# Optimization experiments

Hardware: AMD Instinct MI355X
Metric: run time of the kernel (lower is better)

The kernel has to match this reference:

```python
import jax, jax.numpy as jnp
import numpy as np

N_HEAD = 16
LN_EPS = 1e-5


def _layernorm(x, g, b):
    mu = jnp.mean(x, axis=-1, keepdims=True)
    var = jnp.mean(jnp.square(x - mu), axis=-1, keepdims=True)
    return (x - mu) * jax.lax.rsqrt(var + LN_EPS) * g + b


def setup_inputs() -> dict:
    key = jax.random.key(0)
    ks = jax.random.split(key, 8)
    B, T, C = 2, 2048, 1024
    Dff = 4 * C
    s = 0.02
    return {
        "x": jax.random.normal(ks[0], (B, T, C), jnp.float32),
        "wq": jax.random.normal(ks[1], (C, C), jnp.float32) * s,
        "wk": jax.random.normal(ks[2], (C, C), jnp.float32) * s,
        "wv": jax.random.normal(ks[3], (C, C), jnp.float32) * s,
        "w_proj": jax.random.normal(ks[4], (C, C), jnp.float32) * s,
        "b_proj": jnp.zeros((C,), jnp.float32),
        "w1": jax.random.normal(ks[5], (C, Dff), jnp.float32) * s,
        "b1": jnp.zeros((Dff,), jnp.float32),
        "w2": jax.random.normal(ks[6], (Dff, C), jnp.float32) * s,
        "b2": jnp.zeros((C,), jnp.float32),
        "g1": jnp.ones((C,), jnp.float32),
        "be1": jnp.zeros((C,), jnp.float32),
        "g2": jnp.ones((C,), jnp.float32),
        "be2": jnp.zeros((C,), jnp.float32),
    }


def reference(x, wq, wk, wv, w_proj, b_proj, w1, b1, w2, b2, g1, be1, g2, be2):
    B, T, C = x.shape
    H = N_HEAD
    hd = C // H
    # QKV projections (all heads folded into one matmul each), -> [B,H,T,hd]
    q = (x @ wq).reshape(B, T, H, hd).transpose(0, 2, 1, 3)
    k = (x @ wk).reshape(B, T, H, hd).transpose(0, 2, 1, 3)
    v = (x @ wv).reshape(B, T, H, hd).transpose(0, 2, 1, 3)
    # scaled causal attention; scale = head_size ** -0.5 as in torch source
    scores = jnp.einsum("bhqd,bhkd->bhqk", q, k) * (hd ** -0.5)
    causal = jnp.tril(jnp.ones((T, T), bool))
    scores = jnp.where(causal, scores, jnp.finfo(scores.dtype).min)
    wei = jax.nn.softmax(scores, axis=-1)
    attn = jnp.einsum("bhqk,bhkd->bhqd", wei, v)  # [B,H,T,hd]
    attn = attn.transpose(0, 2, 1, 3).reshape(B, T, C)
    y = attn @ w_proj + b_proj
    # post-LN residuals as in Block.forward
    x = _layernorm(x + y, g1, be1)
    y = jnp.maximum(x @ w1 + b1, 0.0) @ w2 + b2
    x = _layernorm(x + y, g2, be2)
    return x
```

## Files before the change

kernel.cpp:

```cpp
#include <hip/hip_runtime.h>
#include <hip/hip_bf16.h>


typedef __attribute__((ext_vector_type(8))) short bf16x8;
typedef __attribute__((ext_vector_type(4))) float f32x4;
typedef __attribute__((ext_vector_type(4))) short short4v;

__device__ inline short f2bf(float f) {
    __hip_bfloat16 h = __float2bfloat16(f);
    return *reinterpret_cast<short*>(&h);
}
__device__ inline float bf2f(short s) {
    union { unsigned u; float f; } c;
    c.u = ((unsigned)(unsigned short)s) << 16;
    return c.f;
}

__global__ __launch_bounds__(256) void mega_prep(const float* __restrict__ x,
                                                 short* __restrict__ x_bf,
                                                 const float* __restrict__ wq,
                                                 const float* __restrict__ wk,
                                                 const float* __restrict__ wv,
                                                 const float* __restrict__ wp,
                                                 short* __restrict__ wqT,
                                                 short* __restrict__ wkT,
                                                 short* __restrict__ wvT,
                                                 short* __restrict__ wpT,
                                                 const float* __restrict__ w1,
                                                 short* __restrict__ w1T,
                                                 const float* __restrict__ w2,
                                                 short* __restrict__ w2T,
                                                 float scaleq) {
    const int blk = blockIdx.x;
    const int tid = threadIdx.x;
    if (blk < 4096) {
        const int i = blk * 256 + tid;
        float4 v = *(const float4*)(x + (size_t)i * 4);
        short4v o = { f2bf(v.x), f2bf(v.y), f2bf(v.z), f2bf(v.w) };
        *(short4v*)(x_bf + (size_t)i * 4) = o;
        return;
    }
    __shared__ short tile[32][33];
    const int tx = tid & 31, ty = tid >> 5;
    const float* in;
    short* out;
    int R, C, bx, by;
    float scale = 1.0f;
    if (blk < 8192) {
        const int b2 = blk - 4096;
        const int z = b2 >> 10;
        const int rem = b2 & 1023;
        bx = rem & 31; by = rem >> 5;
        R = 1024; C = 1024;
        in = z == 0 ? wq : z == 1 ? wk : z == 2 ? wv : wp;
        out = z == 0 ? wqT : z == 1 ? wkT : z == 2 ? wvT : wpT;
        if (z == 0) scale = scaleq;
    } else if (blk < 12288) {
        const int rem = blk - 8192;
        bx = rem & 127; by = rem >> 7;
        R = 1024; C = 4096;
        in = w1; out = w1T;
    } else {
        const int rem = blk - 12288;
        bx = rem & 31; by = rem >> 5;
        R = 4096; C = 1024;
        in = w2; out = w2T;
    }
    const int c0 = bx * 32, r0 = by * 32;
    for (int i = ty; i < 32; i += 8)
        tile[i][tx] = f2bf(in[(size_t)(r0 + i) * C + c0 + tx] * scale);
    __syncthreads();
    for (int i = ty; i < 32; i += 8)
        out[(size_t)(c0 + i) * R + r0 + tx] = tile[tx][i];
}

template <int BN, int BIAS, int RELU, int OUTBF>
__device__ __forceinline__ void gemm_core(const short* __restrict__ A,
                                          const short* __restrict__ BT,
                                          const float* __restrict__ bias,
                                          void* __restrict__ Cout,
                                          int N, int K, int lda, int ldb,
                                          int gx, int w,
                                          short* As, short* Bs, bool addbias) {
    constexpr int NI = BN / 32;
    const int tid = threadIdx.x;
    const int wid = tid >> 6;
    const int lane = tid & 63;
    const int wr = wid >> 1, wc = wid & 1;
    const int row0 = (w % gx) * 128;
    const int col0 = (w / gx) * BN;
    const int lr = lane & 15;
    const int lk = (lane >> 4) * 8;
    const int sr = lane >> 3;
    const int scs = ((lane & 7) * 8) ^ (sr * 8);
    const int rsw = (lr & 7) * 8;

    f32x4 acc[4][NI] = {};
    for (int k = 0; k < K; k += 64) {
#pragma unroll
        for (int c = 0; c < 4; ++c) {
            const int ch = wid + c * 4;
            const short* ga = A + (size_t)(row0 + ch * 8 + sr) * lda + k + scs;
            __builtin_amdgcn_global_load_lds(
                (const __attribute__((address_space(1))) unsigned int*)ga,
                (__attribute__((address_space(3))) unsigned int*)(As + ch * 512), 16, 0, 0);
        }
#pragma unroll
        for (int c = 0; c < BN / 32; ++c) {
            const int ch = wid + c * 4;
            const short* gb = BT + (size_t)(col0 + ch * 8 + sr) * ldb + k + scs;
            __builtin_amdgcn_global_load_lds(
                (const __attribute__((address_space(1))) unsigned int*)gb,
                (__attribute__((address_space(3))) unsigned int*)(Bs + ch * 512), 16, 0, 0);
        }
        __syncthreads();
#pragma unroll
        for (int kk = 0; kk < 64; kk += 32) {
            const int cof = (kk + lk) ^ rsw;
            bf16x8 a[4], b[NI];
#pragma unroll
            for (int m = 0; m < 4; ++m)
                a[m] = *(const bf16x8*)(As + (wr * 64 + m * 16 + lr) * 64 + cof);
#pragma unroll
            for (int n = 0; n < NI; ++n)
                b[n] = *(const bf16x8*)(Bs + (wc * (BN / 2) + n * 16 + lr) * 64 + cof);
#pragma unroll
            for (int m = 0; m < 4; ++m)
#pragma unroll
                for (int n = 0; n < NI; ++n)
                    acc[m][n] = __builtin_amdgcn_mfma_f32_16x16x32_bf16(a[m], b[n], acc[m][n], 0, 0, 0);
        }
        __syncthreads();
    }
#pragma unroll
    for (int m = 0; m < 4; ++m) {
        int row = row0 + wr * 64 + m * 16 + (lane >> 4) * 4;
#pragma unroll
        for (int n = 0; n < NI; ++n) {
            int col = col0 + wc * (BN / 2) + n * 16 + lr;
            float bv = (BIAS && addbias) ? bias[col] : 0.0f;
#pragma unroll
            for (int r = 0; r < 4; ++r) {
                float v = acc[m][n][r] + bv;
                if (RELU) v = fmaxf(v, 0.0f);
                if (OUTBF)
                    ((short*)Cout)[(size_t)(row + r) * N + col] = f2bf(v);
                else
                    ((float*)Cout)[(size_t)(row + r) * N + col] = v;
            }
        }
    }
}

template <int BN, int BIAS, int RELU, int OUTBF>
__global__ __launch_bounds__(256) void gemm_bt(const short* __restrict__ A,
                                               const short* __restrict__ BT,
                                               const float* __restrict__ bias,
                                               void* __restrict__ Cout,
                                               int N, int K, int lda, int ldb,
                                               void* __restrict__ Cout2) {
    __shared__ short As[128 * 64];
    __shared__ short Bs[BN * 64];
    const int kz = blockIdx.z;
    if (kz) { A += K; BT += K; Cout = Cout2; }
    const int gx = gridDim.x;
    int flat = blockIdx.x + gx * blockIdx.y;
    const int nwg = gx * gridDim.y;
    int w = flat;
    if ((nwg & 7) == 0) {
        const int q = nwg >> 3;
        w = (flat & 7) * q + (flat >> 3);
    }
    gemm_core<BN, BIAS, RELU, OUTBF>(A, BT, bias, Cout, N, K, lda, ldb, gx, w, As, Bs, kz == 0);
}

__global__ __launch_bounds__(256) void gemm_qkv_vt(const short* __restrict__ x_bf,
                                                   const short* __restrict__ wqkT,
                                                   const short* __restrict__ wvT,
                                                   short* __restrict__ qk,
                                                   short* __restrict__ Vt) {
    __shared__ short As[128 * 64];
    __shared__ short Bs[128 * 64];
    int flat = blockIdx.x;
    if (flat < 512) {
        const int w = (flat & 7) * 64 + (flat >> 3);
        gemm_core<128, 0, 0, 1>(x_bf, wqkT, nullptr, qk, 2048, 1024, 1024, 1024, 32, w, As, Bs, false);
    } else {
        flat -= 512;
        const int w = (flat & 7) * 32 + (flat >> 3);
        gemm_core<128, 0, 0, 1>(wvT, x_bf, nullptr, Vt, 4096, 1024, 1024, 1024, 8, w, As, Bs, false);
    }
}

#define ATT_T 2048
#define ATT_QKS 2048
#define ATT_BT 4096

#define LOADK(KF, KB)                                                                     \
    do {                                                                                  \
        const int k0_ = (KB) * 64;                                                        \
        _Pragma("unroll") for (int t = 0; t < 4; ++t) {                                   \
            const size_t krow_ = (size_t)(b * ATT_T + k0_ + 16 * t + lr) * ATT_QKS + h * 64; \
            KF[t][0] = *(const bf16x8*)(Km + krow_ + g * 8);                              \
            KF[t][1] = *(const bf16x8*)(Km + krow_ + 32 + g * 8);                         \
        }                                                                                 \
    } while (0)

#define LOADV(VF, KB)                                                                     \
    do {                                                                                  \
        const int k0_ = (KB) * 64;                                                        \
        _Pragma("unroll") for (int n = 0; n < 4; ++n)                                     \
            _Pragma("unroll") for (int ks = 0; ks < 2; ++ks)                              \
                VF[n][ks] = *(const bf16x8*)(Vt + (size_t)(h * 64 + n * 16 + lr) * ATT_BT + \
                                             b * ATT_T + k0_ + ks * 32 + g * 8);          \
    } while (0)

#define COMPUTE(KF, VF, KB)                                                               \
    do {                                                                                  \
        const int k0_ = (KB) * 64;                                                        \
        const bool edge_ = (KB) == nfull;                                                 \
        _Pragma("unroll") for (int qs = 0; qs < 2; ++qs) {                                \
            f32x4 st[4];                                                                  \
            __builtin_amdgcn_s_setprio(1);                                                \
            _Pragma("unroll") for (int t = 0; t < 4; ++t) {                               \
                f32x4 s = {};                                                             \
                s = __builtin_amdgcn_mfma_f32_16x16x32_bf16(KF[t][0], aq[qs][0], s, 0, 0, 0); \
                s = __builtin_amdgcn_mfma_f32_16x16x32_bf16(KF[t][1], aq[qs][1], s, 0, 0, 0); \
                st[t] = s;                                                                \
            }                                                                             \
            __builtin_amdgcn_s_setprio(0);                                                \
            float rst[4];                                                                 \
            _Pragma("unroll") for (int t = 0; t < 4; ++t) {                               \
                short4v pw;                                                               \
                float pr[4];                                                              \
                _Pragma("unroll") for (int r = 0; r < 4; ++r) {                           \
                    float val = st[t][r];                                                 \
                    if (edge_ && (k0_ + 16 * t + g * 4 + r > qrow[qs])) val = -3e38f;     \
                    float p = exp2f(val);                                                 \
                    pr[r] = p;                                                            \
                    pw[r] = f2bf(p);                                                      \
                }                                                                         \
                rst[t] = (pr[0] + pr[1]) + (pr[2] + pr[3]);                               \
                *(short4v*)(&Plds[wid][qs][lr][16 * t + g * 4]) = pw;                     \
            }                                                                             \
            float rs = (rst[0] + rst[1]) + (rst[2] + rst[3]);                             \
            rs += __shfl_xor(rs, 16);                                                     \
            rs += __shfl_xor(rs, 32);                                                     \
            lrun[qs] += rs;                                                               \
        }                                                                                 \
        asm volatile("s_waitcnt lgkmcnt(0)" ::: "memory");                                \
        __builtin_amdgcn_sched_barrier(0);                                                \
        __builtin_amdgcn_s_setprio(1);                                                    \
        _Pragma("unroll") for (int qs = 0; qs < 2; ++qs)                                  \
            _Pragma("unroll") for (int ks = 0; ks < 2; ++ks) {                            \
                bf16x8 pf = *(const bf16x8*)(&Plds[wid][qs][lr][ks * 32 + g * 8]);        \
                _Pragma("unroll") for (int n = 0; n < 4; ++n)                             \
                    O[qs][n] = __builtin_amdgcn_mfma_f32_16x16x32_bf16(VF[n][ks], pf, O[qs][n], 0, 0, 0); \
            }                                                                             \
        __builtin_amdgcn_s_setprio(0);                                                    \
    } while (0)

__global__ __launch_bounds__(128) void flash_attn(const short* __restrict__ Q,
                                                  const short* __restrict__ Km,
                                                  const short* __restrict__ Vt,
                                                  short* __restrict__ Oout) {
    const int f = blockIdx.x;
    const int wid = threadIdx.x >> 6;
    const int lane = threadIdx.x & 63;
    const int lr = lane & 15;
    const int g = lane >> 4;
    const int xcd = f & 7;
    const int k = f >> 3;
    const int bh = xcd * 4 + (k & 3);
    const int b = bh >> 4;
    const int h = bh & 15;
    const int pair = (k >> 2) * 2 + wid;

    __shared__ __align__(16) short Plds[2][2][16][72];

#pragma unroll 1
    for (int job = 0; job < 2; ++job) {
        const int s = job ? (63 - pair) : pair;
        const int q0 = s << 5;
        const int qrow[2] = { q0 + lr, q0 + 16 + lr };
        const int nfull = s >> 1;

        bf16x8 aq[2][2];
#pragma unroll
        for (int qs = 0; qs < 2; ++qs)
#pragma unroll
            for (int ds = 0; ds < 2; ++ds)
                aq[qs][ds] = *(const bf16x8*)(Q + (size_t)(b * ATT_T + q0 + qs * 16 + lr) * ATT_QKS +
                                              h * 64 + ds * 32 + g * 8);

        f32x4 O[2][4] = {};
        float lrun[2] = { 0.0f, 0.0f };

        bf16x8 kfA[4][2], kfB[4][2], vf[4][2];
        LOADK(kfA, 0);
        int kb = 0;
        while (true) {
            LOADV(vf, kb);
            if (kb < nfull) LOADK(kfB, kb + 1);
            COMPUTE(kfA, vf, kb);
            ++kb;
            if (kb > nfull) break;
            LOADV(vf, kb);
            if (kb < nfull) LOADK(kfA, kb + 1);
            COMPUTE(kfB, vf, kb);
            ++kb;
            if (kb > nfull) break;
        }

#pragma unroll
        for (int qs = 0; qs < 2; ++qs) {
            const float inv = 1.0f / lrun[qs];
#pragma unroll
            for (int n = 0; n < 4; ++n) {
                short4v ov;
#pragma unroll
                for (int r = 0; r < 4; ++r) ov[r] = f2bf(O[qs][n][r] * inv);
                *(short4v*)(Oout + (size_t)(b * ATT_T + q0 + qs * 16 + lr) * 1024 +
                            h * 64 + n * 16 + g * 4) = ov;
            }
        }
    }
}

template <int XB>
__global__ __launch_bounds__(256) void resid_ln(const float* __restrict__ xf,
                                                const short* __restrict__ xb,
                                                const short* __restrict__ y,
                                                const short* __restrict__ yb,
                                                const float* __restrict__ g,
                                                const float* __restrict__ be,
                                                float* __restrict__ of,
                                                short* __restrict__ ob) {
    const int row = blockIdx.x;
    const int tid = threadIdx.x;
    const size_t base = (size_t)row * 1024 + tid * 4;
    float x0, x1, x2, x3;
    if (XB) {
        short4v xv = *(const short4v*)(xb + base);
        x0 = bf2f(xv[0]); x1 = bf2f(xv[1]); x2 = bf2f(xv[2]); x3 = bf2f(xv[3]);
    } else {
        float4 xv = *(const float4*)(xf + base);
        x0 = xv.x; x1 = xv.y; x2 = xv.z; x3 = xv.w;
    }
    short4v yv = *(const short4v*)(y + base);
    float h0 = x0 + bf2f(yv[0]), h1 = x1 + bf2f(yv[1]);
    float h2 = x2 + bf2f(yv[2]), h3 = x3 + bf2f(yv[3]);
    if (yb) {
        short4v bv2 = *(const short4v*)(yb + base);
        h0 += bf2f(bv2[0]); h1 += bf2f(bv2[1]); h2 += bf2f(bv2[2]); h3 += bf2f(bv2[3]);
    }
    float s = h0 + h1 + h2 + h3;
    float ss = h0 * h0 + h1 * h1 + h2 * h2 + h3 * h3;
#pragma unroll
    for (int d = 1; d < 64; d <<= 1) {
        s += __shfl_xor(s, d);
        ss += __shfl_xor(ss, d);
    }
    __shared__ float as_[4], ass_[4];
    if ((tid & 63) == 0) { as_[tid >> 6] = s; ass_[tid >> 6] = ss; }
    __syncthreads();
    s = as_[0] + as_[1] + as_[2] + as_[3];
    ss = ass_[0] + ass_[1] + ass_[2] + ass_[3];
    const float mu = s * (1.0f / 1024.0f);
    const float var = ss * (1.0f / 1024.0f) - mu * mu;
    const float rstd = rsqrtf(var + 1e-5f);
    float4 gv = *(const float4*)(g + tid * 4);
    float4 bv = *(const float4*)(be + tid * 4);
    float o0 = (h0 - mu) * rstd * gv.x + bv.x;
    float o1 = (h1 - mu) * rstd * gv.y + bv.y;
    float o2 = (h2 - mu) * rstd * gv.z + bv.z;
    float o3 = (h3 - mu) * rstd * gv.w + bv.w;
    if (of) {
        float4 ov = { o0, o1, o2, o3 };
        *(float4*)(of + base) = ov;
    }
    if (ob) {
        short4v obv = { f2bf(o0), f2bf(o1), f2bf(o2), f2bf(o3) };
        *(short4v*)(ob + base) = obv;
    }
}


extern "C" void kernel_launch(void* const* d_in, const int* in_sizes, int n_in,
                              void* d_out, int out_size, void* d_ws, size_t ws_size,
                              hipStream_t stream) {
    const float* x = (const float*)d_in[0];
    const float* wq = (const float*)d_in[1];
    const float* wk = (const float*)d_in[2];
    const float* wv = (const float*)d_in[3];
    const float* wp = (const float*)d_in[4];
    const float* bproj = (const float*)d_in[5];
    const float* w1 = (const float*)d_in[6];
    const float* b1 = (const float*)d_in[7];
    const float* w2 = (const float*)d_in[8];
    const float* b2 = (const float*)d_in[9];
    const float* g1 = (const float*)d_in[10];
    const float* be1 = (const float*)d_in[11];
    const float* g2 = (const float*)d_in[12];
    const float* be2 = (const float*)d_in[13];

    char* ws = (char*)d_ws;
    const size_t MB = 1024 * 1024;
    short* x_bf = (short*)(ws + 0);
    short* wqkT = (short*)(ws + 8 * MB);
    short* wqT = wqkT;
    short* wkT = (short*)(ws + 10 * MB);
    short* wvT = (short*)(ws + 12 * MB);
    short* w1T = (short*)(ws + 16 * MB);
    short* w2T = (short*)(ws + 24 * MB);
    short* qk  = (short*)(ws + 32 * MB);
    short* wpT = (short*)(ws + 48 * MB);
    short* Vt  = (short*)(ws + 56 * MB);
    short* hbf = (short*)(ws + 32 * MB);
    short* attn = (short*)(ws + 64 * MB);
    short* x1bf = (short*)(ws + 64 * MB);
    short* y1a = (short*)(ws + 72 * MB);
    short* y1b = (short*)(ws + 0);
    short* y2a = (short*)(ws + 72 * MB);
    short* y2b = (short*)(ws + 0);

    dim3 blk(256);
    const float SC = 0.125f * 1.44269504089f;

    mega_prep<<<dim3(16384), blk, 0, stream>>>(x, x_bf, wq, wk, wv, wp,
                                               wqT, wkT, wvT, wpT,
                                               w1, w1T, w2, w2T, SC);
    gemm_qkv_vt<<<dim3(768), blk, 0, stream>>>(x_bf, wqkT, wvT, qk, Vt);
    flash_attn<<<dim3(512), dim3(128), 0, stream>>>(qk, qk + 1024, Vt, attn);
    gemm_bt<64, 1, 0, 1><<<dim3(32, 16, 2), blk, 0, stream>>>(attn, wpT, bproj, y1a,
                                                              1024, 512, 1024, 1024, y1b);
    resid_ln<0><<<dim3(4096), blk, 0, stream>>>(x, nullptr, y1a, y1b, g1, be1,
                                                nullptr, x1bf);
    gemm_bt<64, 1, 1, 1><<<dim3(32, 64), blk, 0, stream>>>(x1bf, w1T, b1, hbf,
                                                           4096, 1024, 1024, 1024, nullptr);
    gemm_bt<64, 1, 0, 1><<<dim3(32, 16, 2), blk, 0, stream>>>(hbf, w2T, b2, y2a,
                                                              1024, 2048, 4096, 4096, y2b);
    resid_ln<1><<<dim3(4096), blk, 0, stream>>>(nullptr, x1bf, y2a, y2b, g2, be2,
                                                (float*)d_out, nullptr);
}
```

Before: 273.5 us.

## Add dedicated 256x256-tile double-buffered MFMA kernel for MLP first GEMM

```diff
diff --git a/kernel.cpp b/kernel.cpp
--- a/kernel.cpp
+++ b/kernel.cpp
@@ -189,6 +189,108 @@
         flat -= 512;
         const int w = (flat & 7) * 32 + (flat >> 3);
         gemm_core<128, 0, 0, 1>(wvT, x_bf, nullptr, Vt, 4096, 1024, 1024, 1024, 8, w, As, Bs, false);
+    }
+}
+
+#define STAGE_MLP1(KT, BF)                                                                  \
+    do {                                                                                    \
+        const int kof_ = (KT) * 64;                                                         \
+        _Pragma("unroll") for (int l = 0; l < 4; ++l) {                                     \
+            const int ch = wid * 4 + l;                                                     \
+            const short* ga = A + (size_t)(row0 + ch * 8 + sr) * 1024 + kof_ + scs;         \
+            __builtin_amdgcn_global_load_lds(                                               \
+                (const __attribute__((address_space(1))) unsigned int*)ga,                  \
+                (__attribute__((address_space(3))) unsigned int*)(&As[BF][ch * 512]), 16, 0, 0); \
+            const short* gb = BT + (size_t)(col0 + ch * 8 + sr) * 1024 + kof_ + scs;        \
+            __builtin_amdgcn_global_load_lds(                                               \
+                (const __attribute__((address_space(1))) unsigned int*)gb,                  \
+                (__attribute__((address_space(3))) unsigned int*)(&Bs[BF][ch * 512]), 16, 0, 0); \
+        }                                                                                   \
+    } while (0)
+
+__global__ __launch_bounds__(512, 2) void gemm_mlp1(const short* __restrict__ A,
+                                                    const short* __restrict__ BT,
+                                                    const float* __restrict__ bias,
+                                                    short* __restrict__ C) {
+    __shared__ short As[2][256 * 64];
+    __shared__ short Bs[2][256 * 64];
+    const int tid = threadIdx.x;
+    const int wid = tid >> 6;
+    const int lane = tid & 63;
+    const int wm = wid >> 2;
+    const int wn = wid & 3;
+    const int flat = blockIdx.x;
+    const int w = (flat & 7) * 32 + (flat >> 3);
+    const int row0 = (w & 15) * 256;
+    const int col0 = (w >> 4) * 256;
+    const int lr = lane & 15;
+    const int lk = (lane >> 4) * 8;
+    const int sr = lane >> 3;
+    const int scs = ((lane & 7) * 8) ^ (sr * 8);
+    const int rsw = (lr & 7) * 8;
+
+    f32x4 acc[8][4] = {};
+
+    STAGE_MLP1(0, 0);
+    STAGE_MLP1(1, 1);
+
+    const int NK = 16;
+#pragma unroll 1
+    for (int t = 0; t < NK; ++t) {
+        const int c = t & 1;
+        if (t == NK - 1)
+            asm volatile("s_waitcnt vmcnt(0)" ::: "memory");
+        else
+            asm volatile("s_waitcnt vmcnt(8)" ::: "memory");
+        __builtin_amdgcn_s_barrier();
+        bf16x8 bfr[4][2];
+#pragma unroll
+        for (int fj = 0; fj < 4; ++fj)
+#pragma unroll
+            for (int ks = 0; ks < 2; ++ks)
+                bfr[fj][ks] = *(const bf16x8*)(&Bs[c][(wn * 64 + fj * 16 + lr) * 64 +
+                                                      ((ks * 32 + lk) ^ rsw)]);
+#pragma unroll
+        for (int p = 0; p < 4; ++p) {
+            bf16x8 afr[2][2];
+#pragma unroll
+            for (int f = 0; f < 2; ++f)
+#pragma unroll
+                for (int ks = 0; ks < 2; ++ks)
+                    afr[f][ks] = *(const bf16x8*)(&As[c][(wm * 128 + (p * 2 + f) * 16 + lr) * 64 +
+                                                         ((ks * 32 + lk) ^ rsw)]);
+            asm volatile("s_waitcnt lgkmcnt(0)" ::: "memory");
+            __builtin_amdgcn_sched_barrier(0);
+            if (p == 3) {
+                __builtin_amdgcn_s_barrier();
+                if (t + 2 < NK) STAGE_MLP1(t + 2, c);
+            }
+            __builtin_amdgcn_s_setprio(1);
+#pragma unroll
+            for (int f = 0; f < 2; ++f)
+#pragma unroll
+                for (int fj = 0; fj < 4; ++fj)
+#pragma unroll
+                    for (int ks = 0; ks < 2; ++ks)
+                        acc[p * 2 + f][fj] = __builtin_amdgcn_mfma_f32_16x16x32_bf16(
+                            afr[f][ks], bfr[fj][ks], acc[p * 2 + f][fj], 0, 0, 0);
+            __builtin_amdgcn_s_setprio(0);
+            __builtin_amdgcn_s_barrier();
+        }
+    }
+#pragma unroll
+    for (int fi = 0; fi < 8; ++fi) {
+        const int row = row0 + wm * 128 + fi * 16 + (lane >> 4) * 4;
+#pragma unroll
+        for (int fj = 0; fj < 4; ++fj) {
+            const int col = col0 + wn * 64 + fj * 16 + lr;
+            const float bv = bias[col];
+#pragma unroll
+            for (int r = 0; r < 4; ++r) {
+                float v = fmaxf(acc[fi][fj][r] + bv, 0.0f);
+                C[(size_t)(row + r) * 4096 + col] = f2bf(v);
+            }
+        }
     }
 }
 
@@ -436,8 +538,7 @@
                                                               1024, 512, 1024, 1024, y1b);
     resid_ln<0><<<dim3(4096), blk, 0, stream>>>(x, nullptr, y1a, y1b, g1, be1,
                                                 nullptr, x1bf);
-    gemm_bt<64, 1, 1, 1><<<dim3(32, 64), blk, 0, stream>>>(x1bf, w1T, b1, hbf,
-                                                           4096, 1024, 1024, 1024, nullptr);
+    gemm_mlp1<<<dim3(256), dim3(512), 0, stream>>>(x1bf, w1T, b1, hbf);
     gemm_bt<64, 1, 0, 1><<<dim3(32, 16, 2), blk, 0, stream>>>(hbf, w2T, b2, y2a,
                                                               1024, 2048, 4096, 4096, y2b);
     resid_ln<1><<<dim3(4096), blk, 0, stream>>>(nullptr, x1bf, y2a, y2b, g2, be2,
```

After: 266.4 us. -2.6%, faster.
